# Optimization experiments

Hardware: AMD Instinct MI355X
Metric: run time of the kernel (lower is better)

Reference implementation:

```python
import jax, jax.numpy as jnp
import numpy as np

DN = ('NCHW', 'OIHW', 'NCHW')
NUM_DOMAINS = 4


def conv2d(x, w, pad, groups=1):
    return jax.lax.conv_general_dilated(x, w, (1, 1), pad, dimension_numbers=DN,
                                        feature_group_count=groups)


def batchnorm2d(x, w, b, eps=1e-3):
    m = x.mean(axis=(0, 2, 3), keepdims=True)
    v = x.var(axis=(0, 2, 3), keepdims=True)
    return (x - m) / jnp.sqrt(v + eps) * w[None, :, None, None] + b[None, :, None, None]


def avgpool_w(x, k):
    B, C, H, W = x.shape
    Wo = W // k
    return x[..., :Wo * k].reshape(B, C, H, Wo, k).mean(axis=-1)


def mink(u, v):
    # Minkowski inner product <u,v>_L = -u0*v0 + <us,vs>
    return -u[..., 0] * v[..., 0] + (u[..., 1:] * v[..., 1:]).sum(-1)


def lorentz_elu(x):
    s = jax.nn.elu(x[..., 1:])
    t = jnp.sqrt(1.0 + (s * s).sum(-1, keepdims=True))
    return jnp.concatenate([t, s], -1)


def lorentz_avgpool_w(x, k):
    # (B,H,W,C) Lorentz points; window mean then Lorentz centroid projection
    B, H, W, C = x.shape
    Wo = W // k
    s = x[:, :, :Wo * k].reshape(B, H, Wo, k, C).mean(axis=3)
    d = jnp.sqrt(jnp.clip(jnp.abs(mink(s, s)), 1e-8, None))[..., None]
    return s / d


def lorentz_dbn(x, domains, beta, gamma, eps=1e-5):
    # Domain-specific Riemannian batch norm on the Lorentz manifold (k=1),
    # scalar dispersion (Frechet-mean centroid + geodesic variance per domain).
    B, H, W, C = x.shape
    pts = x.reshape(B, H * W, C)
    npts = float(H * W)
    s = jax.ops.segment_sum(pts.sum(axis=1), domains, num_segments=NUM_DOMAINS)  # (D,C)
    cnt = jax.ops.segment_sum(jnp.full((B,), npts, x.dtype), domains, num_segments=NUM_DOMAINS)
    cnt = jnp.maximum(cnt, 1.0)
    s = s / cnt[:, None]
    mu = s / jnp.sqrt(jnp.clip(jnp.abs(mink(s, s)), 1e-8, None))[:, None]  # (D,C) centroids
    mu_b = mu[domains][:, None, :]                                         # (B,1,C)
    ip = mink(mu_b, pts)                                                   # (B,HW)
    dist = jnp.arccosh(jnp.clip(-ip, 1.0 + 1e-7, None))
    u = pts + ip[..., None] * mu_b
    un = jnp.sqrt(jnp.clip(mink(u, u), 1e-8, None))
    v = dist[..., None] * u / un[..., None]                                # log_mu(x)
    var = jax.ops.segment_sum((dist ** 2).sum(axis=1), domains, num_segments=NUM_DOMAINS) / cnt
    o = jnp.zeros((C,), x.dtype).at[0].set(1.0)
    # parallel transport mu -> origin
    v = v + (-v[..., :1]) / (1.0 + mu_b[..., :1]) * (mu_b + o)
    # rescale by gamma / sqrt(var)
    v = v * (gamma / jnp.sqrt(var[domains] + eps))[:, None, None]
    # parallel transport origin -> beta, then expmap at beta
    v = v + (mink(beta, v) / (1.0 + beta[0]))[..., None] * (o + beta)
    vn = jnp.sqrt(jnp.clip(mink(v, v), 1e-8, None))[..., None]
    y = jnp.cosh(vn) * beta + jnp.sinh(vn) * v / vn
    return y.reshape(B, H, W, C)


def setup_inputs() -> dict:
    key = jax.random.key(0)
    ks = jax.random.split(key, 12)
    B = 128
    d = {}
    d['x'] = jax.random.normal(ks[0], (B, 32, 1024), jnp.float32)
    d['domains'] = jax.random.randint(ks[1], (B,), 0, NUM_DOMAINS, jnp.int32)
    d['conv1_w'] = 0.1 * jax.random.normal(ks[2], (16, 1, 1, 32), jnp.float32)
    d['bn1_w'] = jnp.ones((16,), jnp.float32)
    d['bn1_b'] = jnp.zeros((16,), jnp.float32)
    d['dw_w'] = 0.1 * jax.random.normal(ks[3], (32, 1, 32, 1), jnp.float32)
    d['bn2_w'] = jnp.ones((32,), jnp.float32)
    d['bn2_b'] = jnp.zeros((32,), jnp.float32)
    d['ec1_w'] = 0.1 * jax.random.normal(ks[4], (32, 1, 1, 16), jnp.float32)
    d['b2c1_w'] = 0.1 * jax.random.normal(ks[5], (32, 1, 1, 16), jnp.float32)
    d['b2c2_w'] = 0.1 * jax.random.normal(ks[6], (32, 32, 1, 1), jnp.float32)
    d['bn3_w'] = jnp.ones((32,), jnp.float32)
    d['bn3_b'] = jnp.zeros((32,), jnp.float32)
    d['lc1_w'] = 0.2 * jax.random.normal(ks[7], (33, 33), jnp.float32)
    d['bn_beta'] = jnp.zeros((33,), jnp.float32).at[0].set(1.0)
    d['bn_gamma'] = jnp.ones((1,), jnp.float32)
    d['mlr_a'] = 0.1 * jax.random.normal(ks[8], (1,), jnp.float32)
    d['mlr_z'] = 0.1 * jax.random.normal(ks[9], (1, 512), jnp.float32)
    return d


def reference(x, domains, conv1_w, bn1_w, bn1_b, dw_w, bn2_w, bn2_b, ec1_w,
              b2c1_w, b2c2_w, bn3_w, bn3_b, lc1_w, bn_beta, bn_gamma, mlr_a, mlr_z):
    h = x[:, None]                                       # (B,1,32,1024)
    # block1: temporal conv + BN + depthwise spatial conv + BN + ELU + pool
    h = conv2d(h, conv1_w, ((0, 0), (16, 16)))           # (B,16,32,1025)
    h = batchnorm2d(h, bn1_w, bn1_b)
    h = conv2d(h, dw_w, ((0, 0), (0, 0)), groups=16)     # (B,32,1,1025)
    h = batchnorm2d(h, bn2_w, bn2_b)
    h = jax.nn.elu(h)
    h = avgpool_w(h, 4)                                  # (B,32,1,256)
    # ec1 + block2
    h = conv2d(h, ec1_w, ((0, 0), (8, 8)), groups=32)    # (B,32,1,257)
    h = conv2d(h, b2c1_w, ((0, 0), (8, 8)), groups=32)   # (B,32,1,258)
    h = conv2d(h, b2c2_w, ((0, 0), (0, 0)))              # (B,32,1,258)
    h = batchnorm2d(h, bn3_w, bn3_b)
    h = jax.nn.elu(h)
    h = avgpool_w(h, 4)                                  # (B,32,1,64)
    # to Lorentz: permute, L2-normalize, pad time, projx (time = sqrt(1+|s|^2))
    h = jnp.transpose(h, (0, 2, 3, 1))                   # (B,1,64,32)
    h = h / jnp.clip(jnp.linalg.norm(h, axis=-1, keepdims=True), 1e-12, None)
    t = jnp.sqrt(1.0 + (h * h).sum(-1, keepdims=True))
    h = jnp.concatenate([t, h], -1)                      # (B,1,64,33)
    # LorentzConv2d kernel 1 == Lorentz fully-connected: linear then recompute time
    y = jnp.einsum('bhwc,oc->bhwo', h, lc1_w)
    ys = y[..., 1:]
    yt = jnp.sqrt(1.0 + (ys * ys).sum(-1, keepdims=True))
    h = jnp.concatenate([yt, ys], -1)                    # (B,1,64,33)
    h = lorentz_dbn(h, domains, bn_beta, bn_gamma)
    h = lorentz_elu(h)
    h = lorentz_avgpool_w(h, 4)                          # (B,1,16,33)
    # lorentz_flatten: concat spaces, recompute time -> (B, 16*32+1)
    B = h.shape[0]
    fs = h[..., 1:].reshape(B, -1)
    ft = jnp.sqrt(1.0 + (fs * fs).sum(-1, keepdims=True))
    features = jnp.concatenate([ft, fs], -1)             # (B,513)
    # Lorentz MLR (k=1)
    norm_z = jnp.linalg.norm(mlr_z, axis=-1)             # (1,)
    w_t = jnp.sinh(mlr_a) * norm_z
    bet = jnp.sqrt(jnp.clip(-w_t ** 2 + (jnp.cosh(mlr_a) * norm_z) ** 2, 1e-8, None))
    alpha = -w_t * features[:, :1] + jnp.cosh(mlr_a) * (features[:, 1:] @ mlr_z.T)
    dd = jnp.abs(jnp.arcsinh(alpha / bet))
    logits = jnp.sign(alpha) * bet * dd                  # (B,1)
    return logits.squeeze(-1), features
```

## Files before the change

### kernel.cpp

```cpp
#include <hip/hip_runtime.h>
#include <math.h>

#define Bn 128
#define Hh 32
#define Wx 1024

#define N1f 4198400.0f
#define N2f 131200.0f
#define N3f 33024.0f

#define OFF_EH     33
#define OFF_ET     48
#define OFF_G      64
#define OFF_G2     544
#define OFF_A1     1024
#define OFF_B1     1040
#define OFF_S1_3   1056
#define OFF_S2_3   1088
#define OFF_SEG    1120
#define OFF_CNT    1252
#define OFF_DSQ    1256
#define ZERO_N     1280
#define OFF_PC     2048
#define OFF_PS     34816
#define OFF_PD1    35840
#define OFF_PD2    52224
#define OFF_DWOUT  68608
#define OFF_E2     (68608 + 4194304)
#define OFF_C3     OFF_DWOUT
#define OFF_PTS    (OFF_C3 + 1056768)
#define OFF_VO     (OFF_PTS + 270336)

__device__ __forceinline__ float eluf(float x) { return x > 0.f ? x : expm1f(x); }

__global__ __launch_bounds__(256) void k_edge(const float* __restrict__ x,
                                              float* __restrict__ ws) {
    __shared__ float hd[64 * 48];
    __shared__ float tl[64 * 48];
    int tid = threadIdx.x;
    int r0 = blockIdx.x * 64;
    for (int i = tid; i < 64 * 32; i += 256) {
        int r = i >> 5, c = i & 31;
        tl[r * 48 + 16 + c] = 0.f;
    }
#pragma unroll
    for (int it = 0; it < 4; it++) {
        int idx = tid + it * 256;
        int r = idx >> 4, q = idx & 15;
        const float4* base = (const float4*)(x + (r0 + r) * Wx);
        if (q < 12) ((float4*)(hd + r * 48))[q] = base[q];
        else        ((float4*)(tl + r * 48))[q - 12] = base[252 + (q - 12)];
    }
    __syncthreads();
    for (int p = tid; p < 990; p += 256) {
        float acc = 0.f;
        if (p < 480) {
            int d = p / 15, j = p - d * 15;
            for (int r = 0; r < 64; r++) acc += hd[r * 48 + j] * hd[r * 48 + j + d];
            atomicAdd(&ws[OFF_G + p], acc);
        } else if (p < 960) {
            int p2 = p - 480;
            int d = p2 / 15, j = p2 - d * 15;
            for (int r = 0; r < 64; r++) acc += tl[r * 48 + 1 + j] * tl[r * 48 + 1 + j + d];
            atomicAdd(&ws[OFF_G2 + p2], acc);
        } else {
            int j = p - 960;
            if (j < 15) { for (int r = 0; r < 64; r++) acc += hd[r * 48 + j]; }
            else        { for (int r = 0; r < 64; r++) acc += tl[r * 48 + 1 + (j - 15)]; }
            atomicAdd(&ws[OFF_EH + j], acc);
        }
    }
}

__global__ __launch_bounds__(256, 1) void k_corr(const float* __restrict__ x,
                                                 float* __restrict__ ws) {
    __shared__ float xs[2][1060];
    __shared__ float cacc[32];
    __shared__ float sacc;
    int tid = threadIdx.x;
    if (tid < 32) cacc[tid] = 0.f;
    if (tid == 32) sacc = 0.f;
    for (int i = 1024 + tid; i < 1060; i += 256) { xs[0][i] = 0.f; xs[1][i] = 0.f; }
    float acc[32];
#pragma unroll
    for (int d = 0; d < 32; d++) acc[d] = 0.f;
    float sp = 0.f;
    int r0 = blockIdx.x * 4;
    ((float4*)xs[0])[tid] = ((const float4*)(x + r0 * Wx))[tid];
    __syncthreads();
    for (int rr = 0; rr < 4; rr++) {
        float4 nxt;
        if (rr < 3) nxt = ((const float4*)(x + (r0 + rr + 1) * Wx))[tid];
        const float* bq = xs[rr & 1];
        float v[36];
#pragma unroll
        for (int q = 0; q < 9; q++) {
            float4 t4 = ((const float4*)bq)[tid + q];
            v[4 * q] = t4.x; v[4 * q + 1] = t4.y; v[4 * q + 2] = t4.z; v[4 * q + 3] = t4.w;
        }
#pragma unroll
        for (int i = 0; i < 4; i++) {
            sp += v[i];
#pragma unroll
            for (int d = 0; d < 32; d++) acc[d] += v[i] * v[i + d];
        }
        if (rr < 3) ((float4*)xs[(rr + 1) & 1])[tid] = nxt;
        __syncthreads();
    }
    int lane = tid & 63;
#pragma unroll
    for (int d = 0; d < 32; d++) {
        float vv = acc[d];
#pragma unroll
        for (int off = 32; off > 0; off >>= 1) vv += __shfl_down(vv, off);
        if (lane == 0) atomicAdd(&cacc[d], vv);
    }
    {
        float vv = sp;
#pragma unroll
        for (int off = 32; off > 0; off >>= 1) vv += __shfl_down(vv, off);
        if (lane == 0) atomicAdd(&sacc, vv);
    }
    __syncthreads();
    if (tid < 32) ws[OFF_PC + tid * 1024 + blockIdx.x] = cacc[tid];
    if (tid == 32) ws[OFF_PS + blockIdx.x] = sacc;
}

__global__ __launch_bounds__(512) void k_fold(const float* __restrict__ w1,
                                              const float* __restrict__ bn1w,
                                              const float* __restrict__ bn1b,
                                              float* __restrict__ ws) {
    __shared__ float PH[32][16];
    __shared__ float PT[32][16];
    __shared__ float Ts[32];
    __shared__ float w1s[512];
    __shared__ float sumsq[16];
    __shared__ float meanv[16];
    __shared__ float Cs[32];
    __shared__ float sS[16];
    int tid = threadIdx.x;
    w1s[tid] = w1[tid];
    if (tid < 16) sumsq[tid] = 0.f;
    {
        int d = tid >> 4, i = tid & 15;
        const float4* pc = (const float4*)(ws + OFF_PC + d * 1024 + i * 64);
        float s = 0.f;
#pragma unroll
        for (int k = 0; k < 16; k++) { float4 t4 = pc[k]; s += t4.x + t4.y + t4.z + t4.w; }
        s += __shfl_down(s, 8); s += __shfl_down(s, 4);
        s += __shfl_down(s, 2); s += __shfl_down(s, 1);
        if (i == 0) Cs[d] = s;
    }
    __syncthreads();
    if (tid < 32) {
        int d = tid;
        float s = 0.f;
        for (int j = 0; j < 15; j++) { s += ws[OFF_G + d * 15 + j]; PH[d][j] = s; }
        float s2 = 0.f;
        for (int j = 14; j >= 0; j--) { s2 += ws[OFF_G2 + d * 15 + j]; PT[d][j] = s2; }
    } else if (tid < 48) {
        int i = tid - 32;
        const float4* ps = (const float4*)(ws + OFF_PS + i * 64);
        float s = 0.f;
#pragma unroll
        for (int k = 0; k < 16; k++) { float4 t4 = ps[k]; s += t4.x + t4.y + t4.z + t4.w; }
        sS[i] = s;
    }
    __syncthreads();
    if (tid >= 64 && tid < 96) {
        int k = tid - 64;
        float S = 0.f;
        for (int j = 0; j < 16; j++) S += sS[j];
        float t = S;
        for (int j = 0; j <= k - 17; j++) t -= ws[OFF_EH + j];
        if (k <= 14) for (int j = k; j < 15; j++) t -= ws[OFF_ET + j];
        Ts[k] = t;
    }
    __syncthreads();
    int c = tid >> 5, d = tid & 31;
    float Cd = Cs[d];
    float part = 0.f;
    for (int k = 0; k + d < 32; k++) {
        float head = (k >= 17) ? PH[d][k - 17] : 0.f;
        float tail = (k <= 14) ? PT[d][k] : 0.f;
        float R = Cd - head - tail;
        part += w1s[c * 32 + k] * w1s[c * 32 + k + d] * R;
    }
    if (d > 0) part *= 2.f;
    atomicAdd(&sumsq[c], part);
    if (d == 0) {
        float mp = 0.f;
        for (int k = 0; k < 32; k++) mp += w1s[c * 32 + k] * Ts[k];
        meanv[c] = mp / N1f;
    }
    __syncthreads();
    if (tid < 16) {
        float mean = meanv[tid];
        float var = fmaxf(sumsq[tid] / N1f - mean * mean, 0.f);
        float a = bn1w[tid] / sqrtf(var + 1e-3f);
        ws[OFF_A1 + tid] = a;
        ws[OFF_B1 + tid] = bn1b[tid] - mean * a;
    }
}

__global__ __launch_bounds__(256, 1) void k_dw(const float* __restrict__ x,
                                               const float* __restrict__ w1,
                                               const float* __restrict__ dww,
                                               float* __restrict__ ws) {
    __shared__ float dws[256];
    __shared__ float w1s[128];
    __shared__ float Dv[8];
    __shared__ float a1s[4], b1s[4];
    __shared__ float Ys[8 * 296];
    __shared__ float st[16];
    int tid = threadIdx.x;
    int b = blockIdx.x;
    int ocb = blockIdx.y * 8;
    int z = blockIdx.z;
    int wt0 = z * 256;
    int g0 = ocb >> 1;
    dws[tid] = dww[ocb * 32 + tid];
    if (tid < 128) w1s[tid] = w1[g0 * 32 + tid];
    if (tid < 16) st[tid] = 0.f;
    if (tid < 4) { a1s[tid] = ws[OFF_A1 + g0 + tid]; b1s[tid] = ws[OFF_B1 + g0 + tid]; }
    __syncthreads();
    if (tid < 8) {
        float d = 0.f;
        for (int h = 0; h < 32; h++) d += dws[tid * 32 + h];
        Dv[tid] = d;
    }
    for (int p = wt0 + tid; p < wt0 + 288; p += 256) {
        float acc[8];
#pragma unroll
        for (int j = 0; j < 8; j++) acc[j] = 0.f;
        bool inr = (p >= 16 && p < 16 + Wx);
        const float* xb = x + b * (Hh * Wx) + (p - 16);
        for (int h = 0; h < Hh; h++) {
            float xv = inr ? xb[h << 10] : 0.f;
#pragma unroll
            for (int j = 0; j < 8; j++) acc[j] += xv * dws[j * 32 + h];
        }
#pragma unroll
        for (int j = 0; j < 8; j++) Ys[j * 296 + (p - wt0)] = acc[j];
    }
    __syncthreads();
    int w = wt0 + tid;
    int lane = tid & 63;
    for (int jp = 0; jp < 4; jp++) {
        float wr[32];
#pragma unroll
        for (int k = 0; k < 32; k++) wr[k] = w1s[jp * 32 + k];
#pragma unroll
        for (int jj = 0; jj < 2; jj++) {
            int j = jp * 2 + jj;
            float s = 0.f;
#pragma unroll 8
            for (int k = 0; k < 32; k++) s += wr[k] * Ys[j * 296 + tid + k];
            float val = a1s[jp] * s + b1s[jp] * Dv[j];
            ws[OFF_DWOUT + (b * 32 + ocb + j) * 1024 + w] = val;
            float ls1 = val, ls2 = val * val;
            if (z == 3 && tid == 0) {
                float s2 = 0.f;
#pragma unroll
                for (int k = 0; k < 32; k++) s2 += wr[k] * Ys[j * 296 + 256 + k];
                float v2 = a1s[jp] * s2 + b1s[jp] * Dv[j];
                ls1 += v2; ls2 += v2 * v2;
            }
#pragma unroll
            for (int off = 32; off > 0; off >>= 1) {
                ls1 += __shfl_down(ls1, off);
                ls2 += __shfl_down(ls2, off);
            }
            if (lane == 0) { atomicAdd(&st[j], ls1); atomicAdd(&st[8 + j], ls2); }
        }
    }
    __syncthreads();
    if (tid < 8)       ws[OFF_PD1 + (ocb + tid) * 512 + z * 128 + b] = st[tid];
    else if (tid < 16) ws[OFF_PD2 + (ocb + tid - 8) * 512 + z * 128 + b] = st[tid];
}

__global__ __launch_bounds__(64) void k_pe(const float* __restrict__ ec1w,
                                           const float* __restrict__ bc1w,
                                           const float* __restrict__ bn2w,
                                           const float* __restrict__ bn2b,
                                           float* __restrict__ ws) {
    __shared__ float ins[272];
    __shared__ float e1p[288];
    int b = blockIdx.x, c = blockIdx.y;
    int t = threadIdx.x;
    if (t < 8) { ins[t] = 0.f; ins[264 + t] = 0.f; e1p[t] = 0.f; }
    if (t < 23) e1p[265 + t] = 0.f;
    const float4* p1 = (const float4*)(ws + OFF_PD1 + c * 512);
    const float4* p2 = (const float4*)(ws + OFF_PD2 + c * 512);
    float4 a0 = p1[t * 2], a1 = p1[t * 2 + 1], c0 = p2[t * 2], c1 = p2[t * 2 + 1];
    float s1 = a0.x + a0.y + a0.z + a0.w + a1.x + a1.y + a1.z + a1.w;
    float s2 = c0.x + c0.y + c0.z + c0.w + c1.x + c1.y + c1.z + c1.w;
#pragma unroll
    for (int off = 32; off > 0; off >>= 1) {
        s1 += __shfl_xor(s1, off);
        s2 += __shfl_xor(s2, off);
    }
    float mean = s1 / N2f;
    float var = fmaxf(s2 / N2f - mean * mean, 0.f);
    float a = bn2w[c] / sqrtf(var + 1e-3f);
    float bb = bn2b[c] - mean * a;
    const float4* dr = (const float4*)(ws + OFF_DWOUT + (b * 32 + c) * 1024);
#pragma unroll
    for (int q = 0; q < 4; q++) {
        float4 v4 = dr[q * 64 + t];
        ins[8 + q * 64 + t] = 0.25f * (eluf(a * v4.x + bb) + eluf(a * v4.y + bb) +
                                       eluf(a * v4.z + bb) + eluf(a * v4.w + bb));
    }
    __syncthreads();
    float ek[16], bk[16];
#pragma unroll
    for (int k = 0; k < 16; k++) { ek[k] = ec1w[c * 16 + k]; bk[k] = bc1w[c * 16 + k]; }
    for (int w = t; w < 257; w += 64) {
        float s = 0.f;
#pragma unroll
        for (int k = 0; k < 16; k++) s += ins[w + k] * ek[k];
        e1p[8 + w] = s;
    }
    __syncthreads();
    float* e2r = ws + OFF_E2 + (b * 32 + c) * 258;
    for (int w = t; w < 258; w += 64) {
        float s = 0.f;
#pragma unroll
        for (int k = 0; k < 16; k++) s += e1p[w + k] * bk[k];
        e2r[w] = s;
    }
}

__global__ __launch_bounds__(256) void k_sep2(const float* __restrict__ bc2w,
                                              float* __restrict__ ws) {
    __shared__ float es[32 * 129];
    __shared__ float bs[1056];
    int b = blockIdx.x;
    int wb = blockIdx.y * 129;
    int t = threadIdx.x;
    for (int i = t; i < 1024; i += 256) { int o = i >> 5, cc = i & 31; bs[o * 33 + cc] = bc2w[i]; }
    const float* e2b = ws + OFF_E2 + b * 8256;
    for (int i = t; i < 4128; i += 256) {
        int cc = i / 129, wl = i - cc * 129;
        es[i] = e2b[cc * 258 + wb + wl];
    }
    __syncthreads();
    int o = t >> 3, w0 = t & 7;
    float wr[32];
#pragma unroll
    for (int cc = 0; cc < 32; cc++) wr[cc] = bs[o * 33 + cc];
    float s1 = 0.f, s2 = 0.f;
    float* c3r = ws + OFF_C3 + (b * 32 + o) * 258 + wb;
    for (int wl = w0; wl < 129; wl += 8) {
        float s = 0.f;
#pragma unroll
        for (int cc = 0; cc < 32; cc++) s += es[cc * 129 + wl] * wr[cc];
        c3r[wl] = s;
        s1 += s; s2 += s * s;
    }
    s1 += __shfl_down(s1, 4, 8); s1 += __shfl_down(s1, 2, 8); s1 += __shfl_down(s1, 1, 8);
    s2 += __shfl_down(s2, 4, 8); s2 += __shfl_down(s2, 2, 8); s2 += __shfl_down(s2, 1, 8);
    if (w0 == 0) {
        atomicAdd(&ws[OFF_S1_3 + o], s1);
        atomicAdd(&ws[OFF_S2_3 + o], s2);
    }
}

__global__ __launch_bounds__(256, 1) void k_head(const float* __restrict__ bn3w,
                                                 const float* __restrict__ bn3b,
                                                 const float* __restrict__ lc1w,
                                                 const int* __restrict__ domains,
                                                 float* __restrict__ ws) {
    __shared__ float q[2048];
    __shared__ float lc1s[1089];
    __shared__ float psum[33];
    __shared__ float ssyp[4][64];
    __shared__ float a3s[32], b3s[32];
    int tid = threadIdx.x;
    int b = blockIdx.x;
    if (tid < 32) {
        float mean = ws[OFF_S1_3 + tid] / N3f;
        float var = fmaxf(ws[OFF_S2_3 + tid] / N3f - mean * mean, 0.f);
        float a = bn3w[tid] / sqrtf(var + 1e-3f);
        a3s[tid] = a;
        b3s[tid] = bn3b[tid] - mean * a;
    }
    for (int i = tid; i < 1089; i += 256) lc1s[i] = lc1w[i];
    __syncthreads();
    const float* c3 = ws + OFF_C3 + b * 8256;
    for (int idx = tid; idx < 2048; idx += 256) {
        int c = idx >> 6, wp = idx & 63;
        float a = a3s[c], bb = b3s[c];
        float acc = 0.f;
#pragma unroll
        for (int j = 0; j < 4; j++) {
            float e = a * c3[c * 258 + wp * 4 + j] + bb;
            acc += eluf(e);
        }
        q[idx] = 0.25f * acc;
    }
    __syncthreads();
    int w = tid & 63, sub = tid >> 6;
    float qv[32];
    float ssq = 0.f;
#pragma unroll
    for (int c = 0; c < 32; c++) { qv[c] = q[c * 64 + w]; ssq += qv[c] * qv[c]; }
    float inv = 1.f / fmaxf(sqrtf(ssq), 1e-12f);
    float ss2 = 0.f;
#pragma unroll
    for (int c = 0; c < 32; c++) { qv[c] *= inv; ss2 += qv[c] * qv[c]; }
    float t = sqrtf(1.f + ss2);
    int o0 = 1 + sub * 8;
    float p[8];
    float ssy_part = 0.f;
#pragma unroll
    for (int i = 0; i < 8; i++) {
        int o = o0 + i;
        float s = lc1s[o * 33] * t;
#pragma unroll
        for (int c = 0; c < 32; c++) s += lc1s[o * 33 + 1 + c] * qv[c];
        p[i] = s;
        ssy_part += s * s;
    }
    ssyp[sub][w] = ssy_part;
    float* pr = ws + OFF_PTS + (b * 64 + w) * 33;
#pragma unroll
    for (int i = 0; i < 8; i++) pr[o0 + i] = p[i];
    __syncthreads();
    float yt = 0.f;
    if (sub == 0) {
        float ssy = ssyp[0][w] + ssyp[1][w] + ssyp[2][w] + ssyp[3][w];
        yt = sqrtf(1.f + ssy);
        pr[0] = yt;
    }
#pragma unroll
    for (int i = 0; i < 8; i++) {
        float vv = p[i];
#pragma unroll
        for (int off = 32; off > 0; off >>= 1) vv += __shfl_down(vv, off);
        if (w == 0) psum[o0 + i] = vv;
    }
    {
        float vv = yt;
#pragma unroll
        for (int off = 32; off > 0; off >>= 1) vv += __shfl_down(vv, off);
        if (w == 0 && sub == 0) psum[0] = vv;
    }
    __syncthreads();
    int dom = domains[b];
    if (tid < 33) atomicAdd(&ws[OFF_SEG + dom * 33 + tid], psum[tid]);
    if (tid == 64) atomicAdd(&ws[OFF_CNT + dom], 64.f);
}

__global__ __launch_bounds__(64, 1) void k_tangent(const int* __restrict__ domains,
                                                   float* __restrict__ ws) {
    int b = blockIdx.x;
    int w = threadIdx.x;
    int dom = domains[b];
    float cnt = fmaxf(ws[OFF_CNT + dom], 1.f);
    float m[33];
    float s0 = ws[OFF_SEG + dom * 33] / cnt;
    m[0] = s0;
    float msum = 0.f;
#pragma unroll
    for (int c = 1; c < 33; c++) {
        m[c] = ws[OFF_SEG + dom * 33 + c] / cnt;
        msum += m[c] * m[c];
    }
    float mkm = -s0 * s0 + msum;
    float dn = 1.f / sqrtf(fmaxf(fabsf(mkm), 1e-8f));
#pragma unroll
    for (int c = 0; c < 33; c++) m[c] *= dn;
    const float* pr = ws + OFF_PTS + (b * 64 + w) * 33;
    float p[33];
#pragma unroll
    for (int c = 0; c < 33; c++) p[c] = pr[c];
    float ip = -m[0] * p[0];
#pragma unroll
    for (int c = 1; c < 33; c++) ip += m[c] * p[c];
    float z = fmaxf(-ip, 1.f + 1e-7f);
    float dist = acoshf(z);
    float u[33];
#pragma unroll
    for (int c = 0; c < 33; c++) u[c] = p[c] + ip * m[c];
    float mk = -u[0] * u[0];
#pragma unroll
    for (int c = 1; c < 33; c++) mk += u[c] * u[c];
    float un = sqrtf(fmaxf(mk, 1e-8f));
    float r = dist / un;
    float v0 = r * u[0];
    float coef = -v0 / (1.f + m[0]);
    float* vo = ws + OFF_VO + (b * 64 + w) * 33;
    vo[0] = v0 + coef * (m[0] + 1.f);
#pragma unroll
    for (int c = 1; c < 33; c++) vo[c] = r * u[c] + coef * m[c];
    float dsq = dist * dist;
#pragma unroll
    for (int off = 32; off > 0; off >>= 1) dsq += __shfl_down(dsq, off);
    if (w == 0) atomicAdd(&ws[OFF_DSQ + dom], dsq);
}

__global__ __launch_bounds__(64, 1) void k_final(const int* __restrict__ domains,
                                                 const float* __restrict__ beta,
                                                 const float* __restrict__ gamma,
                                                 const float* __restrict__ mlr_a,
                                                 const float* __restrict__ mlr_z,
                                                 float* __restrict__ ws,
                                                 float* __restrict__ out) {
    __shared__ float he[64 * 33];
    __shared__ float hp[16 * 33];
    int b = blockIdx.x;
    int w = threadIdx.x;
    int dom = domains[b];
    float cnt = fmaxf(ws[OFF_CNT + dom], 1.f);
    float var = ws[OFF_DSQ + dom] / cnt;
    float sc = gamma[0] / sqrtf(var + 1e-5f);
    float bt[33];
#pragma unroll
    for (int c = 0; c < 33; c++) bt[c] = beta[c];
    const float* vo = ws + OFF_VO + (b * 64 + w) * 33;
    float v[33];
#pragma unroll
    for (int c = 0; c < 33; c++) v[c] = vo[c] * sc;
    float mb = -bt[0] * v[0];
#pragma unroll
    for (int c = 1; c < 33; c++) mb += bt[c] * v[c];
    float coef = mb / (1.f + bt[0]);
    v[0] += coef * (1.f + bt[0]);
#pragma unroll
    for (int c = 1; c < 33; c++) v[c] += coef * bt[c];
    float mk = -v[0] * v[0];
#pragma unroll
    for (int c = 1; c < 33; c++) mk += v[c] * v[c];
    float vn = sqrtf(fmaxf(mk, 1e-8f));
    float ch = coshf(vn), sh = sinhf(vn) / vn;
    float ss = 0.f;
#pragma unroll
    for (int c = 1; c < 33; c++) {
        float y = ch * bt[c] + sh * v[c];
        float s = eluf(y);
        he[w * 33 + c] = s;
        ss += s * s;
    }
    he[w * 33] = sqrtf(1.f + ss);
    __syncthreads();
    if (w < 16) {
        float tmp[33];
        float mk2;
        {
            float a0 = 0.25f * (he[(4 * w) * 33] + he[(4 * w + 1) * 33] +
                                he[(4 * w + 2) * 33] + he[(4 * w + 3) * 33]);
            tmp[0] = a0;
            mk2 = -a0 * a0;
        }
#pragma unroll
        for (int c = 1; c < 33; c++) {
            float a = 0.25f * (he[(4 * w) * 33 + c] + he[(4 * w + 1) * 33 + c] +
                               he[(4 * w + 2) * 33 + c] + he[(4 * w + 3) * 33 + c]);
            tmp[c] = a;
            mk2 += a * a;
        }
        float dd = sqrtf(fmaxf(fabsf(mk2), 1e-8f));
#pragma unroll
        for (int c = 0; c < 33; c++) hp[w * 33 + c] = tmp[c] / dd;
    }
    __syncthreads();
    float ssq = 0.f, sdz = 0.f, zz = 0.f;
    for (int j = w; j < 512; j += 64) {
        float val = hp[(j >> 5) * 33 + 1 + (j & 31)];
        float zv = mlr_z[j];
        ssq += val * val;
        sdz += val * zv;
        zz += zv * zv;
        out[128 + b * 513 + 1 + j] = val;
    }
#pragma unroll
    for (int off = 32; off > 0; off >>= 1) {
        ssq += __shfl_down(ssq, off);
        sdz += __shfl_down(sdz, off);
        zz += __shfl_down(zz, off);
    }
    if (w == 0) {
        float nz = sqrtf(zz);
        float a = mlr_a[0];
        float cha = coshf(a);
        float wt = sinhf(a) * nz;
        float cn = cha * nz;
        float bet = sqrtf(fmaxf(cn * cn - wt * wt, 1e-8f));
        float ft = sqrtf(1.f + ssq);
        float alpha = -wt * ft + cha * sdz;
        out[128 + b * 513] = ft;
        out[b] = bet * asinhf(alpha / bet);
    }
}

extern "C" void kernel_launch(void* const* d_in, const int* in_sizes, int n_in,
                              void* d_out, int out_size, void* d_ws, size_t ws_size,
                              hipStream_t stream) {
    const float* x       = (const float*)d_in[0];
    const int*   domains = (const int*)d_in[1];
    const float* conv1_w = (const float*)d_in[2];
    const float* bn1_w   = (const float*)d_in[3];
    const float* bn1_b   = (const float*)d_in[4];
    const float* dw_w    = (const float*)d_in[5];
    const float* bn2_w   = (const float*)d_in[6];
    const float* bn2_b   = (const float*)d_in[7];
    const float* ec1_w   = (const float*)d_in[8];
    const float* b2c1_w  = (const float*)d_in[9];
    const float* b2c2_w  = (const float*)d_in[10];
    const float* bn3_w   = (const float*)d_in[11];
    const float* bn3_b   = (const float*)d_in[12];
    const float* lc1_w   = (const float*)d_in[13];
    const float* bn_beta = (const float*)d_in[14];
    const float* bn_gamma= (const float*)d_in[15];
    const float* mlr_a   = (const float*)d_in[16];
    const float* mlr_z   = (const float*)d_in[17];
    float* out = (float*)d_out;
    float* ws  = (float*)d_ws;

    hipMemsetAsync(ws, 0, ZERO_N * sizeof(float), stream);
    k_edge<<<64, 256, 0, stream>>>(x, ws);
    k_corr<<<1024, 256, 0, stream>>>(x, ws);
    k_fold<<<1, 512, 0, stream>>>(conv1_w, bn1_w, bn1_b, ws);
    k_dw<<<dim3(128, 4, 4), 256, 0, stream>>>(x, conv1_w, dw_w, ws);
    k_pe<<<dim3(128, 32), 64, 0, stream>>>(ec1_w, b2c1_w, bn2_w, bn2_b, ws);
    k_sep2<<<dim3(128, 2), 256, 0, stream>>>(b2c2_w, ws);
    k_head<<<Bn, 256, 0, stream>>>(bn3_w, bn3_b, lc1_w, domains, ws);
    k_tangent<<<Bn, 64, 0, stream>>>(domains, ws);
    k_final<<<Bn, 64, 0, stream>>>(domains, bn_beta, bn_gamma, mlr_a, mlr_z, ws, out);
}
```

Measured before the change: 291.3 us.

## Process all channels per block in depthwise kernel with shared input tile

```diff
diff --git a/kernel.cpp b/kernel.cpp
--- a/kernel.cpp
+++ b/kernel.cpp
@@ -203,80 +203,128 @@
     }
 }
 
-__global__ __launch_bounds__(256, 1) void k_dw(const float* __restrict__ x,
+__global__ __launch_bounds__(256, 2) void k_dw(const float* __restrict__ x,
                                                const float* __restrict__ w1,
                                                const float* __restrict__ dww,
                                                float* __restrict__ ws) {
-    __shared__ float dws[256];
-    __shared__ float w1s[128];
-    __shared__ float Dv[8];
-    __shared__ float a1s[4], b1s[4];
-    __shared__ float Ys[8 * 296];
-    __shared__ float st[16];
+    __shared__ float xs[32 * 288];
+    __shared__ float Ys[32 * 288];
+    __shared__ float dws[1024];
+    __shared__ float w1s[512];
+    __shared__ float a1s[16], b1s[16], Dv[32];
     int tid = threadIdx.x;
     int b = blockIdx.x;
-    int ocb = blockIdx.y * 8;
-    int z = blockIdx.z;
+    int z = blockIdx.y;
     int wt0 = z * 256;
-    int g0 = ocb >> 1;
-    dws[tid] = dww[ocb * 32 + tid];
-    if (tid < 128) w1s[tid] = w1[g0 * 32 + tid];
-    if (tid < 16) st[tid] = 0.f;
-    if (tid < 4) { a1s[tid] = ws[OFF_A1 + g0 + tid]; b1s[tid] = ws[OFF_B1 + g0 + tid]; }
-    __syncthreads();
-    if (tid < 8) {
+    for (int i = tid; i < 1024; i += 256) dws[i] = dww[i];
+    w1s[tid] = w1[tid];
+    w1s[256 + tid] = w1[256 + tid];
+    if (tid < 16) { a1s[tid] = ws[OFF_A1 + tid]; b1s[tid] = ws[OFF_B1 + tid]; }
+    const float* xb = x + b * (Hh * Wx);
+    for (int i = tid; i < 32 * 288; i += 256) {
+        int h = i / 288, cc = i - h * 288;
+        int gc = wt0 - 16 + cc;
+        xs[i] = (gc >= 0 && gc < Wx) ? xb[h * Wx + gc] : 0.f;
+    }
+    __syncthreads();
+    if (tid < 32) {
         float d = 0.f;
         for (int h = 0; h < 32; h++) d += dws[tid * 32 + h];
         Dv[tid] = d;
     }
-    for (int p = wt0 + tid; p < wt0 + 288; p += 256) {
-        float acc[8];
-#pragma unroll
-        for (int j = 0; j < 8; j++) acc[j] = 0.f;
-        bool inr = (p >= 16 && p < 16 + Wx);
-        const float* xb = x + b * (Hh * Wx) + (p - 16);
-        for (int h = 0; h < Hh; h++) {
-            float xv = inr ? xb[h << 10] : 0.f;
-#pragma unroll
-            for (int j = 0; j < 8; j++) acc[j] += xv * dws[j * 32 + h];
-        }
-#pragma unroll
-        for (int j = 0; j < 8; j++) Ys[j * 296 + (p - wt0)] = acc[j];
-    }
-    __syncthreads();
-    int w = wt0 + tid;
-    int lane = tid & 63;
-    for (int jp = 0; jp < 4; jp++) {
+#pragma unroll
+    for (int pass = 0; pass < 2; pass++) {
+        int p = pass * 256 + tid;
+        if (p < 288) {
+            float xv[32];
+#pragma unroll
+            for (int h = 0; h < 32; h++) xv[h] = xs[h * 288 + p];
+#pragma unroll
+            for (int ocb = 0; ocb < 4; ocb++) {
+                const float4* d4 = (const float4*)(dws + ocb * 256);
+                float acc[8];
+#pragma unroll
+                for (int j = 0; j < 8; j++) acc[j] = 0.f;
+#pragma unroll
+                for (int j = 0; j < 8; j++) {
+#pragma unroll
+                    for (int hq = 0; hq < 8; hq++) {
+                        float4 dv = d4[j * 8 + hq];
+                        acc[j] += xv[4 * hq] * dv.x + xv[4 * hq + 1] * dv.y +
+                                  xv[4 * hq + 2] * dv.z + xv[4 * hq + 3] * dv.w;
+                    }
+                }
+#pragma unroll
+                for (int j = 0; j < 8; j++) Ys[(ocb * 8 + j) * 288 + p] = acc[j];
+            }
+        }
+    }
+    __syncthreads();
+    int wq = tid & 63;
+    int wave = tid >> 6;
+    int oc0 = wave * 8;
+    float ls1[8], ls2[8];
+#pragma unroll
+    for (int j = 0; j < 8; j++) { ls1[j] = 0.f; ls2[j] = 0.f; }
+#pragma unroll
+    for (int gp = 0; gp < 4; gp++) {
+        int g = wave * 4 + gp;
         float wr[32];
-#pragma unroll
-        for (int k = 0; k < 32; k++) wr[k] = w1s[jp * 32 + k];
+        const float4* wg = (const float4*)(w1s + g * 32);
+#pragma unroll
+        for (int q = 0; q < 8; q++) {
+            float4 t4 = wg[q];
+            wr[4 * q] = t4.x; wr[4 * q + 1] = t4.y; wr[4 * q + 2] = t4.z; wr[4 * q + 3] = t4.w;
+        }
+        float ag = a1s[g], bg = b1s[g];
 #pragma unroll
         for (int jj = 0; jj < 2; jj++) {
-            int j = jp * 2 + jj;
-            float s = 0.f;
-#pragma unroll 8
-            for (int k = 0; k < 32; k++) s += wr[k] * Ys[j * 296 + tid + k];
-            float val = a1s[jp] * s + b1s[jp] * Dv[j];
-            ws[OFF_DWOUT + (b * 32 + ocb + j) * 1024 + w] = val;
-            float ls1 = val, ls2 = val * val;
-            if (z == 3 && tid == 0) {
-                float s2 = 0.f;
-#pragma unroll
-                for (int k = 0; k < 32; k++) s2 += wr[k] * Ys[j * 296 + 256 + k];
-                float v2 = a1s[jp] * s2 + b1s[jp] * Dv[j];
-                ls1 += v2; ls2 += v2 * v2;
+            int j = gp * 2 + jj;
+            int oc = oc0 + j;
+            float y[36];
+            const float4* yq = (const float4*)(Ys + oc * 288 + 4 * wq);
+#pragma unroll
+            for (int q = 0; q < 9; q++) {
+                float4 t4 = yq[q];
+                y[4 * q] = t4.x; y[4 * q + 1] = t4.y; y[4 * q + 2] = t4.z; y[4 * q + 3] = t4.w;
             }
-#pragma unroll
-            for (int off = 32; off > 0; off >>= 1) {
-                ls1 += __shfl_down(ls1, off);
-                ls2 += __shfl_down(ls2, off);
+            float bb = bg * Dv[oc];
+            float ov[4];
+#pragma unroll
+            for (int m = 0; m < 4; m++) {
+                float s = 0.f;
+#pragma unroll
+                for (int k = 0; k < 32; k++) s += wr[k] * y[m + k];
+                float val = ag * s + bb;
+                ov[m] = val;
+                ls1[j] += val; ls2[j] += val * val;
             }
-            if (lane == 0) { atomicAdd(&st[j], ls1); atomicAdd(&st[8 + j], ls2); }
-        }
-    }
-    __syncthreads();
-    if (tid < 8)       ws[OFF_PD1 + (ocb + tid) * 512 + z * 128 + b] = st[tid];
-    else if (tid < 16) ws[OFF_PD2 + (ocb + tid - 8) * 512 + z * 128 + b] = st[tid];
+            *((float4*)(ws + OFF_DWOUT + (b * 32 + oc) * 1024 + wt0 + 4 * wq)) =
+                make_float4(ov[0], ov[1], ov[2], ov[3]);
+            if (z == 3 && wq == 63) {
+                float s = 0.f;
+#pragma unroll
+                for (int k = 0; k < 32; k++) s += wr[k] * Ys[oc * 288 + 256 + k];
+                float val = ag * s + bb;
+                ls1[j] += val; ls2[j] += val * val;
+            }
+        }
+    }
+#pragma unroll
+    for (int j = 0; j < 8; j++) {
+#pragma unroll
+        for (int off = 32; off > 0; off >>= 1) {
+            ls1[j] += __shfl_down(ls1[j], off);
+            ls2[j] += __shfl_down(ls2[j], off);
+        }
+    }
+    if (wq == 0) {
+#pragma unroll
+        for (int j = 0; j < 8; j++) {
+            ws[OFF_PD1 + (oc0 + j) * 512 + z * 128 + b] = ls1[j];
+            ws[OFF_PD2 + (oc0 + j) * 512 + z * 128 + b] = ls2[j];
+        }
+    }
 }
 
 __global__ __launch_bounds__(64) void k_pe(const float* __restrict__ ec1w,
@@ -622,7 +670,7 @@
     k_edge<<<64, 256, 0, stream>>>(x, ws);
     k_corr<<<1024, 256, 0, stream>>>(x, ws);
     k_fold<<<1, 512, 0, stream>>>(conv1_w, bn1_w, bn1_b, ws);
-    k_dw<<<dim3(128, 4, 4), 256, 0, stream>>>(x, conv1_w, dw_w, ws);
+    k_dw<<<dim3(128, 4), 256, 0, stream>>>(x, conv1_w, dw_w, ws);
     k_pe<<<dim3(128, 32), 64, 0, stream>>>(ec1_w, b2c1_w, bn2_w, bn2_b, ws);
     k_sep2<<<dim3(128, 2), 256, 0, stream>>>(b2c2_w, ws);
     k_head<<<Bn, 256, 0, stream>>>(bn3_w, bn3_b, lc1_w, domains, ws);
```

New measurement: 237.1 us. 1.23x faster.
